# Kernel tuning notes

Hardware: AMD Instinct MI355X
Metric: run time of the kernel (lower is better)

## Reference

```python
import jax, jax.numpy as jnp
import numpy as np

N = 100000
E = 1600000
IN_DIM, HID_DIM, OUT_DIM = 128, 64, 40


def setup_inputs() -> dict:
    key = jax.random.key(0)
    k1, k2, k3, k4 = jax.random.split(key, 4)
    x = jax.random.normal(k1, (N, IN_DIM), dtype=jnp.float32)
    edge_index = jax.random.randint(k2, (2, E), 0, N, dtype=jnp.int64)
    W1 = jax.random.normal(k3, (IN_DIM, HID_DIM), dtype=jnp.float32) / np.sqrt(IN_DIM)
    b1 = jnp.zeros((HID_DIM,), dtype=jnp.float32)
    W2 = jax.random.normal(k4, (HID_DIM, OUT_DIM), dtype=jnp.float32) / np.sqrt(HID_DIM)
    b2 = jnp.zeros((OUT_DIM,), dtype=jnp.float32)
    return {"x": x, "edge_index": edge_index, "W1": W1, "b1": b1, "W2": W2, "b2": b2}


def _gcn_conv(x, src, dst, W, b):
    # dense transform first (PyG GCNConv order): [N, out]
    h = x @ W
    n = x.shape[0]
    # symmetric degree normalization with self loops: D^-1/2 (A+I) D^-1/2
    loop = jnp.arange(n, dtype=src.dtype)
    s = jnp.concatenate([src, loop])
    d = jnp.concatenate([dst, loop])
    deg = jax.ops.segment_sum(jnp.ones_like(d, dtype=h.dtype), d, num_segments=n)
    dinv = jnp.where(deg > 0, jax.lax.rsqrt(deg), 0.0)
    norm = dinv[s] * dinv[d]  # [E+N]
    msg = h[s] * norm[:, None]  # gather + scale, [E+N, out]
    out = jax.ops.segment_sum(msg, d, num_segments=n)  # scatter-add
    return out + b


def reference(x, edge_index, W1, b1, W2, b2):
    src, dst = edge_index[0], edge_index[1]
    # dropout is identity in eval mode (training=False)
    h = jax.nn.relu(_gcn_conv(x, src, dst, W1, b1))
    out = _gcn_conv(h, src, dst, W2, b2)
    return out
```

## Files before the change

kernel.cpp:

```cpp
#include <hip/hip_runtime.h>

#define IN_DIM 128
#define HID 64
#define ODIM 40
#define BSH 7
#define BSZ 128
#define NBMAX 1024
#define NBLK 128
#define SCH 2048


__global__ __launch_bounds__(256) void k_hist(const int* __restrict__ dst,
                                              int* __restrict__ histM, int e, int nb) {
    __shared__ int hist[NBMAX];
    const int t = threadIdx.x;
    const int blk = blockIdx.x;
    for (int i = t; i < nb; i += 256) hist[i] = 0;
    __syncthreads();
    const int chunk = (e + NBLK - 1) / NBLK;
    const int beg = blk * chunk, end = min(beg + chunk, e);
    for (int i = beg + t; i < end; i += 256)
        atomicAdd(&hist[dst[i] >> BSH], 1);
    __syncthreads();
    for (int i = t; i < nb; i += 256) histM[i * NBLK + blk] = hist[i];
}


__global__ __launch_bounds__(256) void k_s1(const int* __restrict__ histM,
                                            int* __restrict__ csum, int total) {
    __shared__ int red[256];
    const int t = threadIdx.x;
    const int base = blockIdx.x * SCH + t * 8;
    int s = 0;
#pragma unroll
    for (int j = 0; j < 8; ++j) {
        int idx = base + j;
        if (idx < total) s += histM[idx];
    }
    red[t] = s;
    __syncthreads();
    for (int off = 128; off > 0; off >>= 1) {
        if (t < off) red[t] += red[t + off];
        __syncthreads();
    }
    if (t == 0) csum[blockIdx.x] = red[0];
}

__global__ __launch_bounds__(256) void k_s2(int* __restrict__ csum, int nchunks,
                                            int* __restrict__ rowptr, int n, int e) {
    __shared__ int tmp[256];
    const int tid = threadIdx.x;
    int v = (tid < nchunks) ? csum[tid] : 0;
    tmp[tid] = v;
    __syncthreads();
    for (int off = 1; off < 256; off <<= 1) {
        int t_ = (tid >= off) ? tmp[tid - off] : 0;
        __syncthreads();
        tmp[tid] += t_;
        __syncthreads();
    }
    if (tid < nchunks) csum[tid] = tmp[tid] - v;
    if (tid == 0) rowptr[n] = e;
}

__global__ __launch_bounds__(256) void k_s3(const int* __restrict__ histM,
                                            const int* __restrict__ csum,
                                            int* __restrict__ offM,
                                            int* __restrict__ bbase, int total) {
    __shared__ int tsum[256];
    const int t = threadIdx.x;
    const int base = blockIdx.x * SCH + t * 8;
    int v[8];
#pragma unroll
    for (int j = 0; j < 8; ++j) {
        int idx = base + j;
        v[j] = (idx < total) ? histM[idx] : 0;
    }
    int pre[9];
    pre[0] = 0;
#pragma unroll
    for (int j = 0; j < 8; ++j) pre[j + 1] = pre[j] + v[j];
    tsum[t] = pre[8];
    __syncthreads();
    for (int off = 1; off < 256; off <<= 1) {
        int tv = (t >= off) ? tsum[t - off] : 0;
        __syncthreads();
        tsum[t] += tv;
        __syncthreads();
    }
    const int b0 = csum[blockIdx.x] + (tsum[t] - pre[8]);
#pragma unroll
    for (int j = 0; j < 8; ++j) {
        int idx = base + j;
        if (idx < total) {
            int val = b0 + pre[j];
            offM[idx] = val;
            if ((idx & (NBLK - 1)) == 0) bbase[idx >> 7] = val;
        }
    }
}


__global__ __launch_bounds__(256) void k_bscatter2(const int* __restrict__ src,
                                                   const int* __restrict__ dst,
                                                   const int* __restrict__ offM,
                                                   int* __restrict__ ebuf, int e, int nb) {
    __shared__ int lcur[NBMAX];
    const int t = threadIdx.x;
    const int blk = blockIdx.x;
    for (int i = t; i < nb; i += 256) lcur[i] = offM[i * NBLK + blk];
    __syncthreads();
    const int chunk = (e + NBLK - 1) / NBLK;
    const int beg = blk * chunk, end = min(beg + chunk, e);
    for (int i = beg + t; i < end; i += 256) {
        int s = src[i], d = dst[i];
        int b = d >> BSH;
        int p = atomicAdd(&lcur[b], 1);
        ebuf[p] = s | ((d & (BSZ - 1)) << 20);
    }
}


__global__ __launch_bounds__(256) void k_bsort(const int* __restrict__ ebuf,
                                               const int* __restrict__ bbase,
                                               int* __restrict__ esrc,
                                               int* __restrict__ rowptr,
                                               float* __restrict__ dinv,
                                               int n, int nb, int e) {
    __shared__ int hist[BSZ];
    __shared__ int sc[BSZ];
    __shared__ int hoff[BSZ];
    const int t = threadIdx.x;
    const int b = blockIdx.x;
    const int node0 = b << BSH;
    if (t < BSZ) hist[t] = 0;
    __syncthreads();
    const int beg = bbase[b];
    const int end = (b + 1 < nb) ? bbase[b + 1] : e;
    for (int i = beg + t; i < end; i += 256)
        atomicAdd(&hist[ebuf[i] >> 20], 1);
    __syncthreads();
    int v = (t < BSZ) ? hist[t] : 0;
    if (t < BSZ) sc[t] = v;
    __syncthreads();
    for (int off = 1; off < BSZ; off <<= 1) {
        int add = (t < BSZ && t >= off) ? sc[t - off] : 0;
        __syncthreads();
        if (t < BSZ) sc[t] += add;
        __syncthreads();
    }
    if (t < BSZ) {
        int excl = sc[t] - v;
        hoff[t] = excl;
        int node = node0 + t;
        if (node < n) {
            rowptr[node] = beg + excl;
            dinv[node] = rsqrtf((float)(v + 1));
        }
    }
    __syncthreads();
    for (int i = beg + t; i < end; i += 256) {
        int pk = ebuf[i];
        int dloc = pk >> 20;
        int p = beg + atomicAdd(&hoff[dloc], 1);
        esrc[p] = pk & 0xFFFFF;
    }
}


__global__ __launch_bounds__(256) void k_gemm1(const float* __restrict__ x,
                                               const float* __restrict__ W,
                                               const float* __restrict__ dinv,
                                               float* __restrict__ P, int n) {
    __shared__ float Ws[IN_DIM * HID];
    const int t = threadIdx.x;
    {
        const float4* W4 = (const float4*)W;
        float4* Ws4 = (float4*)Ws;
#pragma unroll
        for (int i = 0; i < 8; ++i) Ws4[t + 256 * i] = W4[t + 256 * i];
    }
    __syncthreads();

    const int row0 = blockIdx.x * 64;
    const int ty = t >> 4, tx = t & 15;
    float acc[4][4];
#pragma unroll
    for (int i = 0; i < 4; ++i)
#pragma unroll
        for (int j = 0; j < 4; ++j) acc[i][j] = 0.f;

    const float4* x4 = (const float4*)x;
    int gr[4];
#pragma unroll
    for (int i = 0; i < 4; ++i) {
        int r = row0 + ty * 4 + i;
        gr[i] = r < n ? r : (n - 1);
    }

#pragma unroll 2
    for (int k = 0; k < IN_DIM; k += 4) {
        float aa[4][4];
#pragma unroll
        for (int i = 0; i < 4; ++i) {
            float4 av = x4[(size_t)gr[i] * 32 + (k >> 2)];
            aa[i][0] = av.x; aa[i][1] = av.y; aa[i][2] = av.z; aa[i][3] = av.w;
        }
#pragma unroll
        for (int q = 0; q < 4; ++q) {
            float4 bv = *(const float4*)&Ws[(k + q) * HID + tx * 4];
#pragma unroll
            for (int i = 0; i < 4; ++i) {
                acc[i][0] = fmaf(aa[i][q], bv.x, acc[i][0]);
                acc[i][1] = fmaf(aa[i][q], bv.y, acc[i][1]);
                acc[i][2] = fmaf(aa[i][q], bv.z, acc[i][2]);
                acc[i][3] = fmaf(aa[i][q], bv.w, acc[i][3]);
            }
        }
    }

#pragma unroll
    for (int i = 0; i < 4; ++i) {
        int r = row0 + ty * 4 + i;
        if (r < n) {
            float s = dinv[r];
            float4 o = make_float4(acc[i][0] * s, acc[i][1] * s, acc[i][2] * s, acc[i][3] * s);
            *(float4*)&P[(size_t)r * HID + tx * 4] = o;
        }
    }
}


__global__ __launch_bounds__(256) void k_gemm2(const float* __restrict__ h,
                                               const float* __restrict__ W,
                                               const float* __restrict__ dinv,
                                               float* __restrict__ P, int n) {
    __shared__ float Ws[HID * 48];
    const int t = threadIdx.x;
#pragma unroll
    for (int i = 0; i < 12; ++i) {
        int idx = t + 256 * i;
        int r = idx / 48, c = idx - r * 48;
        Ws[idx] = (c < ODIM) ? W[r * ODIM + c] : 0.f;
    }
    __syncthreads();

    const int row0 = blockIdx.x * 64;
    const int ty = t >> 4, tx = t & 15;
    float acc[4][3];
#pragma unroll
    for (int i = 0; i < 4; ++i)
#pragma unroll
        for (int j = 0; j < 3; ++j) acc[i][j] = 0.f;

    const float4* h4 = (const float4*)h;
    int gr[4];
#pragma unroll
    for (int i = 0; i < 4; ++i) {
        int r = row0 + ty * 4 + i;
        gr[i] = r < n ? r : (n - 1);
    }

#pragma unroll 2
    for (int k = 0; k < HID; k += 4) {
        float aa[4][4];
#pragma unroll
        for (int i = 0; i < 4; ++i) {
            float4 av = h4[(size_t)gr[i] * 16 + (k >> 2)];
            aa[i][0] = av.x; aa[i][1] = av.y; aa[i][2] = av.z; aa[i][3] = av.w;
        }
#pragma unroll
        for (int q = 0; q < 4; ++q) {
            const float* wr = &Ws[(k + q) * 48 + tx * 3];
            float b0 = wr[0], b1v = wr[1], b2v = wr[2];
#pragma unroll
            for (int i = 0; i < 4; ++i) {
                acc[i][0] = fmaf(aa[i][q], b0, acc[i][0]);
                acc[i][1] = fmaf(aa[i][q], b1v, acc[i][1]);
                acc[i][2] = fmaf(aa[i][q], b2v, acc[i][2]);
            }
        }
    }

#pragma unroll
    for (int i = 0; i < 4; ++i) {
        int r = row0 + ty * 4 + i;
        if (r < n) {
            float s = dinv[r];
#pragma unroll
            for (int j = 0; j < 3; ++j) {
                int c = tx * 3 + j;
                if (c < ODIM) P[(size_t)r * ODIM + c] = acc[i][j] * s;
            }
        }
    }
}


__global__ __launch_bounds__(256) void k_agg1(const int* __restrict__ rowptr,
                                              const int* __restrict__ esrc,
                                              const float4* __restrict__ P4,
                                              const float* __restrict__ dinv,
                                              const float* __restrict__ b,
                                              float4* __restrict__ h4, int n) {
    const int t = threadIdx.x;
    const int lane = t & 63;
    const int node = blockIdx.x * 4 + (t >> 6);
    if (node >= n) return;
    const int grp = lane >> 4, q = lane & 15;
    const int beg = rowptr[node], end = rowptr[node + 1];

    float4 acc = make_float4(0.f, 0.f, 0.f, 0.f);
    int j = beg;
#pragma unroll 4
    for (; j + 3 < end; j += 4) {
        int s = esrc[j + grp];
        float4 v = P4[(size_t)s * 16 + q];
        acc.x += v.x; acc.y += v.y; acc.z += v.z; acc.w += v.w;
    }
    if (j + grp < end) {
        int s = esrc[j + grp];
        float4 v = P4[(size_t)s * 16 + q];
        acc.x += v.x; acc.y += v.y; acc.z += v.z; acc.w += v.w;
    }
    acc.x += __shfl_xor(acc.x, 16); acc.y += __shfl_xor(acc.y, 16);
    acc.z += __shfl_xor(acc.z, 16); acc.w += __shfl_xor(acc.w, 16);
    acc.x += __shfl_xor(acc.x, 32); acc.y += __shfl_xor(acc.y, 32);
    acc.z += __shfl_xor(acc.z, 32); acc.w += __shfl_xor(acc.w, 32);

    if (grp == 0) {
        float4 self = P4[(size_t)node * 16 + q];
        float di = dinv[node];
        float4 bb = *(const float4*)&b[q * 4];
        float4 r;
        r.x = fmaxf(fmaf(di, acc.x + self.x, bb.x), 0.f);
        r.y = fmaxf(fmaf(di, acc.y + self.y, bb.y), 0.f);
        r.z = fmaxf(fmaf(di, acc.z + self.z, bb.z), 0.f);
        r.w = fmaxf(fmaf(di, acc.w + self.w, bb.w), 0.f);
        h4[(size_t)node * 16 + q] = r;
    }
}


__global__ __launch_bounds__(256) void k_agg2(const int* __restrict__ rowptr,
                                              const int* __restrict__ esrc,
                                              const float4* __restrict__ P4,
                                              const float* __restrict__ dinv,
                                              const float* __restrict__ b,
                                              float4* __restrict__ out4, int n) {
    const int t = threadIdx.x;
    const int lane = t & 63;
    const int node = blockIdx.x * 4 + (t >> 6);
    if (node >= n) return;
    const int grp = lane / 10;
    const int q = lane - grp * 10;
    const bool act = grp < 6;
    const int beg = rowptr[node], end = rowptr[node + 1];

    float4 acc = make_float4(0.f, 0.f, 0.f, 0.f);
    int j = beg;
#pragma unroll 4
    for (; j + 5 < end; j += 6) {
        if (act) {
            int s = esrc[j + grp];
            float4 v = P4[(size_t)s * 10 + q];
            acc.x += v.x; acc.y += v.y; acc.z += v.z; acc.w += v.w;
        }
    }
    if (act && j + grp < end) {
        int s = esrc[j + grp];
        float4 v = P4[(size_t)s * 10 + q];
        acc.x += v.x; acc.y += v.y; acc.z += v.z; acc.w += v.w;
    }

    {
        float tx_ = __shfl(acc.x, lane + 30), ty_ = __shfl(acc.y, lane + 30);
        float tz_ = __shfl(acc.z, lane + 30), tw_ = __shfl(acc.w, lane + 30);
        if (lane < 30) { acc.x += tx_; acc.y += ty_; acc.z += tz_; acc.w += tw_; }
    }
    {
        float tx_ = __shfl(acc.x, lane + 20), ty_ = __shfl(acc.y, lane + 20);
        float tz_ = __shfl(acc.z, lane + 20), tw_ = __shfl(acc.w, lane + 20);
        if (lane < 10) { acc.x += tx_; acc.y += ty_; acc.z += tz_; acc.w += tw_; }
    }
    {
        float tx_ = __shfl(acc.x, lane + 10), ty_ = __shfl(acc.y, lane + 10);
        float tz_ = __shfl(acc.z, lane + 10), tw_ = __shfl(acc.w, lane + 10);
        if (lane < 10) { acc.x += tx_; acc.y += ty_; acc.z += tz_; acc.w += tw_; }
    }

    if (lane < 10) {
        float4 self = P4[(size_t)node * 10 + q];
        float di = dinv[node];
        float4 bb = *(const float4*)&b[q * 4];
        float4 r;
        r.x = fmaf(di, acc.x + self.x, bb.x);
        r.y = fmaf(di, acc.y + self.y, bb.y);
        r.z = fmaf(di, acc.z + self.z, bb.z);
        r.w = fmaf(di, acc.w + self.w, bb.w);
        out4[(size_t)node * 10 + q] = r;
    }
}


extern "C" void kernel_launch(void* const* d_in, const int* in_sizes, int n_in,
                              void* d_out, int out_size, void* d_ws, size_t ws_size,
                              hipStream_t stream) {
    const float* x  = (const float*)d_in[0];
    const int*   ei = (const int*)d_in[1];
    const float* W1 = (const float*)d_in[2];
    const float* b1 = (const float*)d_in[3];
    const float* W2 = (const float*)d_in[4];
    const float* b2 = (const float*)d_in[5];

    const int n = in_sizes[0] / IN_DIM;
    const int e = in_sizes[1] / 2;
    const int* src = ei;
    const int* dst = ei + e;
    const int nb = (n + BSZ - 1) >> BSH;
    const int total = nb * NBLK;
    const int nchunks = (total + SCH - 1) / SCH;

    auto align = [](size_t b) { return (b + 255) & ~(size_t)255; };
    char* ws = (char*)d_ws;
    size_t o = 0;
    int*   histM = (int*)(ws + o);   o += align((size_t)NBMAX * NBLK * 4);
    int*   offM  = (int*)(ws + o);   o += align((size_t)NBMAX * NBLK * 4);
    int*   csum  = (int*)(ws + o);   o += align((size_t)256 * 4);
    int*   bbase = (int*)(ws + o);   o += align((size_t)NBMAX * 4);
    float* dinv  = (float*)(ws + o); o += align((size_t)n * 4);
    int*   rowptr= (int*)(ws + o);   o += align((size_t)(n + 1) * 4);
    int*   ebuf  = (int*)(ws + o);   o += align((size_t)e * 4);
    int*   esrc  = (int*)(ws + o);   o += align((size_t)e * 4);
    float* P1    = (float*)(ws + o); o += align((size_t)n * HID * 4);
    float* h     = (float*)(ws + o); o += align((size_t)n * HID * 4);

    float* out = (float*)d_out;

    k_hist<<<NBLK, 256, 0, stream>>>(dst, histM, e, nb);
    k_s1<<<nchunks, 256, 0, stream>>>(histM, csum, total);
    k_s2<<<1, 256, 0, stream>>>(csum, nchunks, rowptr, n, e);
    k_s3<<<nchunks, 256, 0, stream>>>(histM, csum, offM, bbase, total);
    k_bscatter2<<<NBLK, 256, 0, stream>>>(src, dst, offM, ebuf, e, nb);
    k_bsort<<<nb, 256, 0, stream>>>(ebuf, bbase, esrc, rowptr, dinv, n, nb, e);

    k_gemm1<<<(n + 63) / 64, 256, 0, stream>>>(x, W1, dinv, P1, n);
    k_agg1<<<(n + 3) / 4, 256, 0, stream>>>(rowptr, esrc, (const float4*)P1, dinv, b1,
                                            (float4*)h, n);

    k_gemm2<<<(n + 63) / 64, 256, 0, stream>>>(h, W2, dinv, P1, n);
    k_agg2<<<(n + 3) / 4, 256, 0, stream>>>(rowptr, esrc, (const float4*)P1, dinv, b2,
                                            (float4*)out, n);
}
```

Baseline: 337.4 us.

## Fuse second-layer GEMM into first aggregation and double histogram block count

The layer-1 aggregation kernel now keeps each node's post-ReLU hidden row in shared memory. It then immediately multiplies that row by W2, scaled by dinv, to write the layer-2 projection. This removes the separate gemm2 kernel and the global write and re-read of the hidden activation buffer. Separately, the number of edge-partition blocks in the histogram and scatter phase goes from 128 to 256, for more parallelism in the bucket sort. In exchange, the fused epilogue is a per-thread scalar 64-term dot product that reads W2 from global memory and adds a block-wide barrier to the aggregation kernel.

```diff
diff --git a/kernel.cpp b/kernel.cpp
--- a/kernel.cpp
+++ b/kernel.cpp
@@ -6,7 +6,8 @@
 #define BSH 7
 #define BSZ 128
 #define NBMAX 1024
-#define NBLK 128
+#define NBLK 256
+#define NBLKSH 8
 #define SCH 2048
 
 
@@ -95,7 +96,7 @@
         if (idx < total) {
             int val = b0 + pre[j];
             offM[idx] = val;
-            if ((idx & (NBLK - 1)) == 0) bbase[idx >> 7] = val;
+            if ((idx & (NBLK - 1)) == 0) bbase[idx >> NBLKSH] = val;
         }
     }
 }
@@ -231,84 +232,22 @@
 }
 
 
-__global__ __launch_bounds__(256) void k_gemm2(const float* __restrict__ h,
-                                               const float* __restrict__ W,
+__global__ __launch_bounds__(256) void k_agg1f(const int* __restrict__ rowptr,
+                                               const int* __restrict__ esrc,
+                                               const float4* __restrict__ P4,
                                                const float* __restrict__ dinv,
-                                               float* __restrict__ P, int n) {
-    __shared__ float Ws[HID * 48];
-    const int t = threadIdx.x;
-#pragma unroll
-    for (int i = 0; i < 12; ++i) {
-        int idx = t + 256 * i;
-        int r = idx / 48, c = idx - r * 48;
-        Ws[idx] = (c < ODIM) ? W[r * ODIM + c] : 0.f;
-    }
-    __syncthreads();
-
-    const int row0 = blockIdx.x * 64;
-    const int ty = t >> 4, tx = t & 15;
-    float acc[4][3];
-#pragma unroll
-    for (int i = 0; i < 4; ++i)
-#pragma unroll
-        for (int j = 0; j < 3; ++j) acc[i][j] = 0.f;
-
-    const float4* h4 = (const float4*)h;
-    int gr[4];
-#pragma unroll
-    for (int i = 0; i < 4; ++i) {
-        int r = row0 + ty * 4 + i;
-        gr[i] = r < n ? r : (n - 1);
-    }
-
-#pragma unroll 2
-    for (int k = 0; k < HID; k += 4) {
-        float aa[4][4];
-#pragma unroll
-        for (int i = 0; i < 4; ++i) {
-            float4 av = h4[(size_t)gr[i] * 16 + (k >> 2)];
-            aa[i][0] = av.x; aa[i][1] = av.y; aa[i][2] = av.z; aa[i][3] = av.w;
-        }
-#pragma unroll
-        for (int q = 0; q < 4; ++q) {
-            const float* wr = &Ws[(k + q) * 48 + tx * 3];
-            float b0 = wr[0], b1v = wr[1], b2v = wr[2];
-#pragma unroll
-            for (int i = 0; i < 4; ++i) {
-                acc[i][0] = fmaf(aa[i][q], b0, acc[i][0]);
-                acc[i][1] = fmaf(aa[i][q], b1v, acc[i][1]);
-                acc[i][2] = fmaf(aa[i][q], b2v, acc[i][2]);
-            }
-        }
-    }
-
-#pragma unroll
-    for (int i = 0; i < 4; ++i) {
-        int r = row0 + ty * 4 + i;
-        if (r < n) {
-            float s = dinv[r];
-#pragma unroll
-            for (int j = 0; j < 3; ++j) {
-                int c = tx * 3 + j;
-                if (c < ODIM) P[(size_t)r * ODIM + c] = acc[i][j] * s;
-            }
-        }
-    }
-}
-
-
-__global__ __launch_bounds__(256) void k_agg1(const int* __restrict__ rowptr,
-                                              const int* __restrict__ esrc,
-                                              const float4* __restrict__ P4,
-                                              const float* __restrict__ dinv,
-                                              const float* __restrict__ b,
-                                              float4* __restrict__ h4, int n) {
+                                               const float* __restrict__ b1,
+                                               const float* __restrict__ W2,
+                                               float* __restrict__ P2, int n) {
+    __shared__ float hrow[4][HID];
     const int t = threadIdx.x;
     const int lane = t & 63;
-    const int node = blockIdx.x * 4 + (t >> 6);
-    if (node >= n) return;
+    const int w = t >> 6;
+    const int node0 = blockIdx.x * 4;
+    int node = node0 + w;
+    const int nodec = node < n ? node : (n - 1);
     const int grp = lane >> 4, q = lane & 15;
-    const int beg = rowptr[node], end = rowptr[node + 1];
+    const int beg = rowptr[nodec], end = rowptr[nodec + 1];
 
     float4 acc = make_float4(0.f, 0.f, 0.f, 0.f);
     int j = beg;
@@ -329,15 +268,27 @@
     acc.z += __shfl_xor(acc.z, 32); acc.w += __shfl_xor(acc.w, 32);
 
     if (grp == 0) {
-        float4 self = P4[(size_t)node * 16 + q];
-        float di = dinv[node];
-        float4 bb = *(const float4*)&b[q * 4];
+        float4 self = P4[(size_t)nodec * 16 + q];
+        float di = dinv[nodec];
+        float4 bb = *(const float4*)&b1[q * 4];
         float4 r;
         r.x = fmaxf(fmaf(di, acc.x + self.x, bb.x), 0.f);
         r.y = fmaxf(fmaf(di, acc.y + self.y, bb.y), 0.f);
         r.z = fmaxf(fmaf(di, acc.z + self.z, bb.z), 0.f);
         r.w = fmaxf(fmaf(di, acc.w + self.w, bb.w), 0.f);
-        h4[(size_t)node * 16 + q] = r;
+        *(float4*)&hrow[w][q * 4] = r;
+    }
+    __syncthreads();
+
+    if (t < 4 * ODIM) {
+        const int local = t / ODIM, c = t - local * ODIM;
+        int pn = node0 + local;
+        if (pn < n) {
+            float s = 0.f;
+#pragma unroll
+            for (int k = 0; k < HID; ++k) s = fmaf(hrow[local][k], W2[k * ODIM + c], s);
+            P2[(size_t)pn * ODIM + c] = s * dinv[pn];
+        }
     }
 }
 
@@ -433,7 +384,7 @@
     int*   ebuf  = (int*)(ws + o);   o += align((size_t)e * 4);
     int*   esrc  = (int*)(ws + o);   o += align((size_t)e * 4);
     float* P1    = (float*)(ws + o); o += align((size_t)n * HID * 4);
-    float* h     = (float*)(ws + o); o += align((size_t)n * HID * 4);
+    float* P2    = (float*)(ws + o); o += align((size_t)n * ODIM * 4);
 
     float* out = (float*)d_out;
 
@@ -445,10 +396,10 @@
     k_bsort<<<nb, 256, 0, stream>>>(ebuf, bbase, esrc, rowptr, dinv, n, nb, e);
 
     k_gemm1<<<(n + 63) / 64, 256, 0, stream>>>(x, W1, dinv, P1, n);
-    k_agg1<<<(n + 3) / 4, 256, 0, stream>>>(rowptr, esrc, (const float4*)P1, dinv, b1,
-                                            (float4*)h, n);
-
-    k_gemm2<<<(n + 63) / 64, 256, 0, stream>>>(h, W2, dinv, P1, n);
-    k_agg2<<<(n + 3) / 4, 256, 0, stream>>>(rowptr, esrc, (const float4*)P1, dinv, b2,
+
+    k_agg1f<<<(n + 3) / 4, 256, 0, stream>>>(rowptr, esrc, (const float4*)P1, dinv, b1,
+                                             W2, P2, n);
+
+    k_agg2<<<(n + 3) / 4, 256, 0, stream>>>(rowptr, esrc, (const float4*)P2, dinv, b2,
                                             (float4*)out, n);
 }
```

After: 330.3 us. 1.02x faster.
